# Performance work log

Measured on AMD Instinct MI355X. Metric: run time of the kernel, lower is better.

Reference implementation:

```python
import jax, jax.numpy as jnp
import numpy as np

NUM_FRAME = 300
LEN_FRAME = 512


def setup_inputs() -> dict:
    key = jax.random.key(0)
    # nervegram: [batch, freq, time, channel]
    nervegram = jax.random.normal(key, (4, 50, 20000, 2), dtype=jnp.float32)
    return {"nervegram": nervegram}


def reference(nervegram):
    # [B, F, T, C] -> [B, F, C, T]
    x = jnp.transpose(nervegram.astype(jnp.float32), (0, 1, 3, 2))
    T = x.shape[-1]

    # frame start indices (static, matches np.linspace(..., dtype=int))
    starts = np.linspace(0, T - LEN_FRAME, NUM_FRAME).astype(np.int64)
    idx = starts[:, None] + np.arange(LEN_FRAME)  # [NUM_FRAME, LEN_FRAME]
    frames = x[..., idx]  # [B, F, C, NUM_FRAME, LEN_FRAME]

    # periodic Hann window (tf.signal.hann_window, periodic=True)
    n = jnp.arange(LEN_FRAME, dtype=jnp.float32)
    window = 0.5 - 0.5 * jnp.cos(2.0 * jnp.pi * n / LEN_FRAME)
    frames = frames * window

    # Wiener-Khinchin autocorrelation: irfft(|rfft(x)|^2)
    spec = jnp.fft.rfft(frames, axis=-1)
    acf = jnp.fft.irfft(spec * jnp.conj(spec), n=LEN_FRAME, axis=-1)
    acf = jax.nn.relu(acf)

    # normalize by sqrt of zero-lag value (guard zeros)
    norm = acf[..., 0:1]
    norm = jnp.where(norm == 0, jnp.ones_like(norm), norm)
    acf = acf / jnp.sqrt(norm)

    # one_sided: keep non-negative lags
    acf = acf[..., : LEN_FRAME // 2]  # [B, F, C, NUM_FRAME, LAGS]

    # channel_mode == 'mean': [B, F, NUM_FRAME, C, LAGS] -> mean over C
    acf = jnp.transpose(acf, (0, 1, 3, 2, 4))
    acf = jnp.mean(acf, axis=-2)  # [B, F, NUM_FRAME, LAGS]
    return acf
```

## Files before the change

### kernel.cpp

```cpp
#include <hip/hip_runtime.h>

#define NUM_FRAME 300
#define LEN_FRAME 512
#define T_LEN     20000

typedef float floatx4 __attribute__((ext_vector_type(4)));
typedef int   int2a   __attribute__((ext_vector_type(2), aligned(4)));
typedef unsigned int uint32;
typedef long long i64;

#define A1_OFF  756
#define B_OFF   1512
#define B_STR   544
#define PAIR8   3696
#define SCR_OFF (4 * PAIR8)

struct alignas(16) WinTab {
    float w[512];
    constexpr WinTab() : w{} {
        for (int n = 0; n < 512; ++n) {
            int mm = (n <= 256) ? n : 512 - n;
            double x = 3.14159265358979323846 * (double)mm / 512.0;
            double t = x, s = x, x2 = x * x;
            for (int i = 1; i <= 10; ++i) { t *= -x2 / (double)((2 * i) * (2 * i + 1)); s += t; }
            w[n] = (float)(32.0 * s * s);
        }
    }
};
__device__ const WinTab wtab{};

__global__ __launch_bounds__(256, 8) void acorr_fp8(const float* __restrict__ in,
                                                    float* __restrict__ out) {
    __shared__ __align__(16) char lds8[4 * PAIR8 + 2112];

    const int tid = threadIdx.x;
    const int fj = tid >> 7;
    const int m  = tid & 127;
    const int x0 = 4 * m;

    int   dreg[2];
    char* Pc[2];

    {
        const int G  = blockIdx.x * 2 + fj;
        const int bc = (int)((unsigned)G / (unsigned)NUM_FRAME);
        const int fr = G - bc * NUM_FRAME;
        const int start = (int)(((unsigned)fr * (unsigned)(T_LEN - LEN_FRAME))
                                / (unsigned)(NUM_FRAME - 1));
        const float2* src = (const float2*)(in + (size_t)2 * ((size_t)bc * T_LEN + start));

        const floatx4 wv = *(const floatx4*)&wtab.w[x0];
        const float2 v0 = src[x0], v1 = src[x0 + 1], v2 = src[x0 + 2], v3 = src[x0 + 3];

        #pragma unroll
        for (int c = 0; c < 2; ++c) {
            float f0 = (c ? v0.y : v0.x) * wv[0];
            float f1 = (c ? v1.y : v1.x) * wv[1];
            float f2 = (c ? v2.y : v2.x) * wv[2];
            float f3 = (c ? v3.y : v3.x) * wv[3];
            int d0 = __builtin_amdgcn_cvt_pk_fp8_f32(f0, f1, 0,  false);
            d0     = __builtin_amdgcn_cvt_pk_fp8_f32(f2, f3, d0, true);

            char* P = &lds8[(fj * 2 + c) * PAIR8];
            Pc[c]   = P;
            dreg[c] = d0;
            *(int*)(P + x0 + 240)          = d0;
            *(int*)(P + A1_OFF + x0 + 240) = d0;
            if (x0 >= 272) {
                *(int*)(P + x0 - 272)          = d0;
                *(int*)(P + A1_OFF + x0 - 272) = d0;
            }
        }
    }
    __syncthreads();

    {
        const int nbo = 240 + ((x0 + 4) & 511);
        #pragma unroll
        for (int c = 0; c < 2; ++c) {
            char* P = Pc[c];
            const int d0 = dreg[c];
            const int d1 = *(const int*)(P + nbo);
            #pragma unroll
            for (int s = 0; s < 4; ++s) {
                int dsv = (s == 0) ? d0
                        : (int)__builtin_amdgcn_alignbyte((uint32)d1, (uint32)d0, (uint32)s);
                *(int*)(P + B_OFF + B_STR * s + x0) = dsv;
                if (x0 < 16)
                    *(int*)(P + B_OFF + B_STR * s + x0 + 512) = dsv;
            }
        }
    }
    __syncthreads();

    const int w    = tid >> 6;
    const int lane = tid & 63;
    const int il   = lane & 15;
    const int q    = lane >> 4;

    const char* P  = &lds8[w * PAIR8];
    const char* aP = P + (240 + 8 * q - 16 * il) + ((il & 8) ? A1_OFF : 0);
    const char* bP = P + B_OFF + B_STR * (il & 3) + 8 * q + 4 * (il >> 2);

    floatx4 acc = {0.f, 0.f, 0.f, 0.f};
    #pragma unroll
    for (int u = 0; u < 16; ++u) {
        int2a av = *(const int2a*)(aP + 32 * u);
        int2a bv = *(const int2a*)(bP + 32 * u);
        acc = __builtin_amdgcn_mfma_f32_16x16x32_fp8_fp8(
            __builtin_bit_cast(i64, av), __builtin_bit_cast(i64, bv), acc, 0, 0, 0);
    }

    float n0  = __shfl(acc[0], 0, 64);
    float n0r = fmaxf(n0, 0.f);
    float inv = (n0r == 0.f) ? (1.0f / 1024.0f) : (rsqrtf(n0r) * (1.0f / 32.0f));
    float r0 = fmaxf(acc[0], 0.f) * inv;
    float r1 = fmaxf(acc[1], 0.f) * inv;
    float r2 = fmaxf(acc[2], 0.f) * inv;
    float r3 = fmaxf(acc[3], 0.f) * inv;

    float* scr = (float*)&lds8[SCR_OFF];
    const int f   = w >> 1;
    const int idx = f * 264 + q * 65 + il;
    if (w & 1) {
        scr[idx +  0] = r0; scr[idx + 16] = r1;
        scr[idx + 32] = r2; scr[idx + 48] = r3;
    }
    __syncthreads();
    if (!(w & 1)) {
        const int G = blockIdx.x * 2 + f;
        float* ob = out + (size_t)G * 256 + q * 64 + il;
        ob[ 0] = 0.5f * (r0 + scr[idx +  0]);
        ob[16] = 0.5f * (r1 + scr[idx + 16]);
        ob[32] = 0.5f * (r2 + scr[idx + 32]);
        ob[48] = 0.5f * (r3 + scr[idx + 48]);
    }
}

extern "C" void kernel_launch(void* const* d_in, const int* in_sizes, int n_in,
                              void* d_out, int out_size, void* d_ws, size_t ws_size,
                              hipStream_t stream) {
    const float* in = (const float*)d_in[0];
    float* out = (float*)d_out;
    dim3 grid(30000);
    dim3 block(256);
    acorr_fp8<<<grid, block, 0, stream>>>(in, out);
}
```

Measured before the change: 124.2 us.

## Use 16x16x128 scaled FP8 MFMA with one wave per frame, both channels

Switches from 16 small 16x16x32 FP8 MFMAs to 4 larger 16x16x128 scaled MFMAs per channel. Each wave now handles one frame and both channels, so the LDS scratch exchange and one barrier go away, and the two channels are averaged in registers. Each thread loads 8 samples plus 4 neighbours directly, which lets it build the shifted B copies without a second LDS pass and barrier. Four frames are processed per block, halving the grid. LDS per block grows and the launch-bounds occupancy hint drops from 8 to 6.

```diff
diff --git a/kernel.cpp b/kernel.cpp
--- a/kernel.cpp
+++ b/kernel.cpp
@@ -5,15 +5,15 @@
 #define T_LEN     20000
 
 typedef float floatx4 __attribute__((ext_vector_type(4)));
+typedef int   intx4   __attribute__((ext_vector_type(4)));
+typedef int   intx8   __attribute__((ext_vector_type(8)));
 typedef int   int2a   __attribute__((ext_vector_type(2), aligned(4)));
+typedef int   int2w   __attribute__((ext_vector_type(2)));
 typedef unsigned int uint32;
-typedef long long i64;
 
-#define A1_OFF  756
-#define B_OFF   1512
-#define B_STR   544
-#define PAIR8   3696
-#define SCR_OFF (4 * PAIR8)
+#define B_OFF  752
+#define B_STR  560
+#define PAIR8  2992
 
 struct alignas(16) WinTab {
     float w[512];
@@ -29,112 +29,125 @@
 };
 __device__ const WinTab wtab{};
 
-__global__ __launch_bounds__(256, 8) void acorr_fp8(const float* __restrict__ in,
+__global__ __launch_bounds__(256, 6) void acorr_fp8(const float* __restrict__ in,
                                                     float* __restrict__ out) {
-    __shared__ __align__(16) char lds8[4 * PAIR8 + 2112];
+    __shared__ __align__(16) char lds8[8 * PAIR8];
 
     const int tid = threadIdx.x;
-    const int fj = tid >> 7;
-    const int m  = tid & 127;
-    const int x0 = 4 * m;
-
-    int   dreg[2];
-    char* Pc[2];
+    const int fj  = tid >> 6;
+    const int m   = tid & 63;
+    const int x0  = 8 * m;
 
     {
-        const int G  = blockIdx.x * 2 + fj;
+        const int G  = blockIdx.x * 4 + fj;
         const int bc = (int)((unsigned)G / (unsigned)NUM_FRAME);
         const int fr = G - bc * NUM_FRAME;
         const int start = (int)(((unsigned)fr * (unsigned)(T_LEN - LEN_FRAME))
                                 / (unsigned)(NUM_FRAME - 1));
         const float2* src = (const float2*)(in + (size_t)2 * ((size_t)bc * T_LEN + start));
 
-        const floatx4 wv = *(const floatx4*)&wtab.w[x0];
-        const float2 v0 = src[x0], v1 = src[x0 + 1], v2 = src[x0 + 2], v3 = src[x0 + 3];
+        const int cn = (x0 + 8) & 511;
+
+        const float2 v0 = src[x0],     v1 = src[x0 + 1], v2 = src[x0 + 2], v3 = src[x0 + 3];
+        const float2 v4 = src[x0 + 4], v5 = src[x0 + 5], v6 = src[x0 + 6], v7 = src[x0 + 7];
+        const float2 c0 = src[cn],     c1 = src[cn + 1], c2 = src[cn + 2], c3 = src[cn + 3];
+
+        const floatx4 wva = *(const floatx4*)&wtab.w[x0];
+        const floatx4 wvb = *(const floatx4*)&wtab.w[x0 + 4];
+        const floatx4 wvc = *(const floatx4*)&wtab.w[cn];
 
         #pragma unroll
         for (int c = 0; c < 2; ++c) {
-            float f0 = (c ? v0.y : v0.x) * wv[0];
-            float f1 = (c ? v1.y : v1.x) * wv[1];
-            float f2 = (c ? v2.y : v2.x) * wv[2];
-            float f3 = (c ? v3.y : v3.x) * wv[3];
+            float f0 = (c ? v0.y : v0.x) * wva[0];
+            float f1 = (c ? v1.y : v1.x) * wva[1];
+            float f2 = (c ? v2.y : v2.x) * wva[2];
+            float f3 = (c ? v3.y : v3.x) * wva[3];
+            float f4 = (c ? v4.y : v4.x) * wvb[0];
+            float f5 = (c ? v5.y : v5.x) * wvb[1];
+            float f6 = (c ? v6.y : v6.x) * wvb[2];
+            float f7 = (c ? v7.y : v7.x) * wvb[3];
+            float g0 = (c ? c0.y : c0.x) * wvc[0];
+            float g1 = (c ? c1.y : c1.x) * wvc[1];
+            float g2 = (c ? c2.y : c2.x) * wvc[2];
+            float g3 = (c ? c3.y : c3.x) * wvc[3];
+
             int d0 = __builtin_amdgcn_cvt_pk_fp8_f32(f0, f1, 0,  false);
             d0     = __builtin_amdgcn_cvt_pk_fp8_f32(f2, f3, d0, true);
+            int d1 = __builtin_amdgcn_cvt_pk_fp8_f32(f4, f5, 0,  false);
+            d1     = __builtin_amdgcn_cvt_pk_fp8_f32(f6, f7, d1, true);
+            int d2 = __builtin_amdgcn_cvt_pk_fp8_f32(g0, g1, 0,  false);
+            d2     = __builtin_amdgcn_cvt_pk_fp8_f32(g2, g3, d2, true);
 
             char* P = &lds8[(fj * 2 + c) * PAIR8];
-            Pc[c]   = P;
-            dreg[c] = d0;
-            *(int*)(P + x0 + 240)          = d0;
-            *(int*)(P + A1_OFF + x0 + 240) = d0;
-            if (x0 >= 272) {
-                *(int*)(P + x0 - 272)          = d0;
-                *(int*)(P + A1_OFF + x0 - 272) = d0;
+            *(int2w*)(P + 240 + x0) = (int2w){d0, d1};
+            if (x0 >= 272)
+                *(int2w*)(P + x0 - 272) = (int2w){d0, d1};
+            #pragma unroll
+            for (int s = 0; s < 4; ++s) {
+                int e0 = (s == 0) ? d0
+                       : (int)__builtin_amdgcn_alignbyte((uint32)d1, (uint32)d0, (uint32)s);
+                int e1 = (s == 0) ? d1
+                       : (int)__builtin_amdgcn_alignbyte((uint32)d2, (uint32)d1, (uint32)s);
+                *(int2w*)(P + B_OFF + B_STR * s + x0) = (int2w){e0, e1};
+                if (x0 < 16)
+                    *(int2w*)(P + B_OFF + B_STR * s + x0 + 512) = (int2w){e0, e1};
             }
         }
     }
     __syncthreads();
 
-    {
-        const int nbo = 240 + ((x0 + 4) & 511);
-        #pragma unroll
-        for (int c = 0; c < 2; ++c) {
-            char* P = Pc[c];
-            const int d0 = dreg[c];
-            const int d1 = *(const int*)(P + nbo);
-            #pragma unroll
-            for (int s = 0; s < 4; ++s) {
-                int dsv = (s == 0) ? d0
-                        : (int)__builtin_amdgcn_alignbyte((uint32)d1, (uint32)d0, (uint32)s);
-                *(int*)(P + B_OFF + B_STR * s + x0) = dsv;
-                if (x0 < 16)
-                    *(int*)(P + B_OFF + B_STR * s + x0 + 512) = dsv;
-            }
-        }
-    }
-    __syncthreads();
-
-    const int w    = tid >> 6;
     const int lane = tid & 63;
     const int il   = lane & 15;
     const int q    = lane >> 4;
 
-    const char* P  = &lds8[w * PAIR8];
-    const char* aP = P + (240 + 8 * q - 16 * il) + ((il & 8) ? A1_OFF : 0);
-    const char* bP = P + B_OFF + B_STR * (il & 3) + 8 * q + 4 * (il >> 2);
+    const char* P0 = &lds8[(fj * 2) * PAIR8];
+    const char* aP = P0 + (240 - 16 * il + 32 * q);
+    const char* bP = P0 + B_OFF + B_STR * (il & 3) + 4 * (il >> 2) + 32 * q;
 
-    floatx4 acc = {0.f, 0.f, 0.f, 0.f};
+    floatx4 acc0 = {0.f, 0.f, 0.f, 0.f};
+    floatx4 acc1 = {0.f, 0.f, 0.f, 0.f};
     #pragma unroll
-    for (int u = 0; u < 16; ++u) {
-        int2a av = *(const int2a*)(aP + 32 * u);
-        int2a bv = *(const int2a*)(bP + 32 * u);
-        acc = __builtin_amdgcn_mfma_f32_16x16x32_fp8_fp8(
-            __builtin_bit_cast(i64, av), __builtin_bit_cast(i64, bv), acc, 0, 0, 0);
+    for (int u = 0; u < 4; ++u) {
+        const int o = 128 * u;
+        {
+            intx4 al = *(const intx4*)(aP + o);
+            intx4 ah = *(const intx4*)(aP + o + 16);
+            int2a b0 = *(const int2a*)(bP + o);
+            int2a b1 = *(const int2a*)(bP + o + 8);
+            int2a b2 = *(const int2a*)(bP + o + 16);
+            int2a b3 = *(const int2a*)(bP + o + 24);
+            intx8 a = {al.x, al.y, al.z, al.w, ah.x, ah.y, ah.z, ah.w};
+            intx8 b = {b0.x, b0.y, b1.x, b1.y, b2.x, b2.y, b3.x, b3.y};
+            acc0 = __builtin_amdgcn_mfma_scale_f32_16x16x128_f8f6f4(
+                a, b, acc0, 0, 0, 0, 0x7F7F7F7F, 0, 0x7F7F7F7F);
+        }
+        {
+            intx4 al = *(const intx4*)(aP + PAIR8 + o);
+            intx4 ah = *(const intx4*)(aP + PAIR8 + o + 16);
+            int2a b0 = *(const int2a*)(bP + PAIR8 + o);
+            int2a b1 = *(const int2a*)(bP + PAIR8 + o + 8);
+            int2a b2 = *(const int2a*)(bP + PAIR8 + o + 16);
+            int2a b3 = *(const int2a*)(bP + PAIR8 + o + 24);
+            intx8 a = {al.x, al.y, al.z, al.w, ah.x, ah.y, ah.z, ah.w};
+            intx8 b = {b0.x, b0.y, b1.x, b1.y, b2.x, b2.y, b3.x, b3.y};
+            acc1 = __builtin_amdgcn_mfma_scale_f32_16x16x128_f8f6f4(
+                a, b, acc1, 0, 0, 0, 0x7F7F7F7F, 0, 0x7F7F7F7F);
+        }
     }
 
-    float n0  = __shfl(acc[0], 0, 64);
-    float n0r = fmaxf(n0, 0.f);
-    float inv = (n0r == 0.f) ? (1.0f / 1024.0f) : (rsqrtf(n0r) * (1.0f / 32.0f));
-    float r0 = fmaxf(acc[0], 0.f) * inv;
-    float r1 = fmaxf(acc[1], 0.f) * inv;
-    float r2 = fmaxf(acc[2], 0.f) * inv;
-    float r3 = fmaxf(acc[3], 0.f) * inv;
+    float n00 = __int_as_float(__builtin_amdgcn_readfirstlane(__float_as_int(acc0[0])));
+    float n01 = __int_as_float(__builtin_amdgcn_readfirstlane(__float_as_int(acc1[0])));
+    float n0r0 = fmaxf(n00, 0.f);
+    float n0r1 = fmaxf(n01, 0.f);
+    float inv0 = (n0r0 == 0.f) ? (1.0f / 1024.0f) : (rsqrtf(n0r0) * (1.0f / 32.0f));
+    float inv1 = (n0r1 == 0.f) ? (1.0f / 1024.0f) : (rsqrtf(n0r1) * (1.0f / 32.0f));
 
-    float* scr = (float*)&lds8[SCR_OFF];
-    const int f   = w >> 1;
-    const int idx = f * 264 + q * 65 + il;
-    if (w & 1) {
-        scr[idx +  0] = r0; scr[idx + 16] = r1;
-        scr[idx + 32] = r2; scr[idx + 48] = r3;
-    }
-    __syncthreads();
-    if (!(w & 1)) {
-        const int G = blockIdx.x * 2 + f;
-        float* ob = out + (size_t)G * 256 + q * 64 + il;
-        ob[ 0] = 0.5f * (r0 + scr[idx +  0]);
-        ob[16] = 0.5f * (r1 + scr[idx + 16]);
-        ob[32] = 0.5f * (r2 + scr[idx + 32]);
-        ob[48] = 0.5f * (r3 + scr[idx + 48]);
-    }
+    const int G = blockIdx.x * 4 + fj;
+    float* ob = out + (size_t)G * 256 + q * 64 + il;
+    ob[ 0] = 0.5f * (fmaxf(acc0[0], 0.f) * inv0 + fmaxf(acc1[0], 0.f) * inv1);
+    ob[16] = 0.5f * (fmaxf(acc0[1], 0.f) * inv0 + fmaxf(acc1[1], 0.f) * inv1);
+    ob[32] = 0.5f * (fmaxf(acc0[2], 0.f) * inv0 + fmaxf(acc1[2], 0.f) * inv1);
+    ob[48] = 0.5f * (fmaxf(acc0[3], 0.f) * inv0 + fmaxf(acc1[3], 0.f) * inv1);
 }
 
 extern "C" void kernel_launch(void* const* d_in, const int* in_sizes, int n_in,
@@ -142,7 +155,7 @@
                               hipStream_t stream) {
     const float* in = (const float*)d_in[0];
     float* out = (float*)d_out;
-    dim3 grid(30000);
+    dim3 grid(15000);
     dim3 block(256);
     acorr_fp8<<<grid, block, 0, stream>>>(in, out);
 }
```

New measurement: 120.8 us. -2.7%, faster.
